# Performance work log

Measured on AMD Instinct MI355X. Metric: run time of the kernel, lower is better.

## Reference

```python
import jax, jax.numpy as jnp
import numpy as np

N_EMBD = 768
N_HEAD = 12
HEAD_DIM = N_EMBD // N_HEAD


def setup_inputs() -> dict:
    key = jax.random.key(0)
    k0, k1, k2, k3, k4 = jax.random.split(key, 5)
    B, T, C = 2, 4096, N_EMBD
    x = jax.random.normal(k0, (B, T, C), dtype=jnp.float32)
    # c_attn: Linear(C, 3C); c_proj: Linear(C, C). torch Linear: y = x @ W.T + b
    s = 1.0 / np.sqrt(C)
    W_attn = jax.random.uniform(k1, (3 * C, C), dtype=jnp.float32, minval=-s, maxval=s)
    b_attn = jax.random.uniform(k2, (3 * C,), dtype=jnp.float32, minval=-s, maxval=s)
    W_proj = jax.random.uniform(k3, (C, C), dtype=jnp.float32, minval=-s, maxval=s)
    b_proj = jax.random.uniform(k4, (C,), dtype=jnp.float32, minval=-s, maxval=s)
    return {"x": x, "W_attn": W_attn, "b_attn": b_attn, "W_proj": W_proj, "b_proj": b_proj}


def reference(x, W_attn, b_attn, W_proj, b_proj):
    B, T, C = x.shape
    H, D = N_HEAD, HEAD_DIM
    qkv = x @ W_attn.T + b_attn                      # [B,T,3C]
    q, k, v = jnp.split(qkv, 3, axis=-1)
    # [B,T,C] -> [B,H,T,D]
    q = q.reshape(B, T, H, D).transpose(0, 2, 1, 3)
    k = k.reshape(B, T, H, D).transpose(0, 2, 1, 3)
    v = v.reshape(B, T, H, D).transpose(0, 2, 1, 3)
    scale = 1.0 / jnp.sqrt(jnp.asarray(D, dtype=x.dtype))
    att = jnp.einsum('bhqd,bhkd->bhqk', q, k) * scale  # [B,H,T,T]
    att = jax.nn.softmax(att, axis=-1)
    y = jnp.einsum('bhqk,bhkd->bhqd', att, v)          # [B,H,T,D]
    y = y.transpose(0, 2, 1, 3).reshape(B, T, C)
    return y @ W_proj.T + b_proj
```

## Files before the change

### kernel.cpp

```cpp
#include <hip/hip_runtime.h>
#include <stdint.h>
#include <stddef.h>

typedef __bf16 bf16_t;
typedef bf16_t bf16x4 __attribute__((ext_vector_type(4)));
typedef bf16_t bf16x8 __attribute__((ext_vector_type(8)));
typedef float  f32x4  __attribute__((ext_vector_type(4)));
typedef _Float16 f16_t;
typedef f16_t f16x2 __attribute__((ext_vector_type(2)));
typedef f16_t f16x4 __attribute__((ext_vector_type(4)));
typedef f16_t f16x8 __attribute__((ext_vector_type(8)));
typedef __fp16 fp16x2_raw __attribute__((ext_vector_type(2)));

__device__ __forceinline__ f16x2 pkrtz(float a, float b) {
    fp16x2_raw r = __builtin_amdgcn_cvt_pkrtz(a, b);
    union { fp16x2_raw r; f16x2 h; } u;
    u.r = r;
    return u.h;
}

#define MFMA_BF16_K32(a, b, c) __builtin_amdgcn_mfma_f32_16x16x32_bf16(a, b, c, 0, 0, 0)
#define MFMA_F16_K32(a, b, c)  __builtin_amdgcn_mfma_f32_16x16x32_f16(a, b, c, 0, 0, 0)

__device__ __forceinline__ void gload_lds16(const void* g, void* l) {
    __builtin_amdgcn_global_load_lds(
        (const __attribute__((address_space(1))) void*)g,
        (__attribute__((address_space(3))) void*)l,
        16, 0, 0);
}

#define NX 1572864
#define NWA 442368
#define NWP 147456
__global__ void cvt_all(const float* __restrict__ x, const float* __restrict__ Wa,
                        const float* __restrict__ Wp, bf16_t* __restrict__ xb,
                        bf16_t* __restrict__ Wab, bf16_t* __restrict__ Wpb) {
    int i = blockIdx.x * blockDim.x + threadIdx.x;
    const float4* src; bf16_t* dst; int j;
    if (i < NX)            { src = (const float4*)x;  dst = xb;  j = i; }
    else if (i < NX + NWA) { src = (const float4*)Wa; dst = Wab; j = i - NX; }
    else                   { src = (const float4*)Wp; dst = Wpb; j = i - NX - NWA; }
    float4 f = src[j];
    bf16x4 o = { (bf16_t)f.x, (bf16_t)f.y, (bf16_t)f.z, (bf16_t)f.w };
    ((bf16x4*)dst)[j] = o;
}

template <int KDIM>
__device__ __forceinline__ void gemm_mainloop(
    const bf16_t* __restrict__ A, const bf16_t* __restrict__ Bt,
    bf16_t* As, bf16_t* Bs, int m0, int n0, int wave, int lane, f32x4 acc[4][4])
{
    const int quad = lane >> 4, l15 = lane & 15;
    const int wm = ((wave >> 1) << 6), wn = ((wave & 1) << 6);

    const int srow = (wave << 4) + (lane >> 2);
    const int sw   = (((lane & 3) ^ ((srow >> 1) & 3)) << 3);
    const bf16_t* gA = A  + (size_t)(m0 + srow) * KDIM + sw;
    const bf16_t* gB = Bt + (size_t)(n0 + srow) * KDIM + sw;
    bf16_t* lA0 = As + wave * 512;
    bf16_t* lA1 = As + 2048 + wave * 512;
    bf16_t* lB0 = Bs + wave * 512;
    bf16_t* lB1 = Bs + 2048 + wave * 512;

    const int xorv = ((quad ^ ((l15 >> 1) & 3)) << 3);

    for (int k0 = 0; k0 < KDIM; k0 += 32) {
        __syncthreads();
        gload_lds16(gA + k0,                       lA0);
        gload_lds16(gA + (size_t)64 * KDIM + k0,   lA1);
        gload_lds16(gB + k0,                       lB0);
        gload_lds16(gB + (size_t)64 * KDIM + k0,   lB1);
        __syncthreads();

        bf16x8 af[4], bfr[4];
#pragma unroll
        for (int t = 0; t < 4; t++) {
            af[t]  = *(const bf16x8*)(As + (wm + t * 16 + l15) * 32 + xorv);
            bfr[t] = *(const bf16x8*)(Bs + (wn + t * 16 + l15) * 32 + xorv);
        }
#pragma unroll
        for (int mt = 0; mt < 4; mt++)
#pragma unroll
            for (int nt = 0; nt < 4; nt++)
                acc[mt][nt] = MFMA_BF16_K32(af[mt], bfr[nt], acc[mt][nt]);
    }
}

__global__ __launch_bounds__(256) void gemm_qkv(
    const bf16_t* __restrict__ A,
    const bf16_t* __restrict__ Bt,
    const float* __restrict__ bias,
    bf16_t* __restrict__ qo, bf16_t* __restrict__ ko, f16_t* __restrict__ vo)
{
    __shared__ bf16_t As[128 * 32];
    __shared__ bf16_t Bs[128 * 32];
    const int tid = threadIdx.x, wave = tid >> 6, lane = tid & 63;
    const int quad = lane >> 4, l15 = lane & 15;
    const int m0 = blockIdx.y * 128, n0 = blockIdx.x * 128;
    f32x4 acc[4][4] = {};
    gemm_mainloop<768>(A, Bt, As, Bs, m0, n0, wave, lane, acc);

    const int wm = ((wave >> 1) << 6), wn = ((wave & 1) << 6);
#pragma unroll
    for (int nt = 0; nt < 4; nt++) {
        const int cc = n0 + wn + nt * 16 + l15;
        const float bia = bias[cc];
        const int which = cc / 768;
        const int rem = cc - which * 768;
        const int h = rem >> 6, d = rem & 63;
        if (which < 2) {
            bf16_t* dst = (which == 0) ? qo : ko;
#pragma unroll
            for (int mt = 0; mt < 4; mt++) {
#pragma unroll
                for (int r = 0; r < 4; r++) {
                    const int row = m0 + wm + mt * 16 + quad * 4 + r;
                    const int b = row >> 12, t = row & 4095;
                    dst[((size_t)(b * 12 + h) * 4096 + t) * 64 + d] =
                        (bf16_t)(acc[mt][nt][r] + bia);
                }
            }
        } else {
#pragma unroll
            for (int mt = 0; mt < 4; mt++) {
                const int row0 = m0 + wm + mt * 16 + quad * 4;
                const int b = row0 >> 12, t0 = row0 & 4095;
                f16x4 ov = { (f16_t)(acc[mt][nt][0] + bia),
                             (f16_t)(acc[mt][nt][1] + bia),
                             (f16_t)(acc[mt][nt][2] + bia),
                             (f16_t)(acc[mt][nt][3] + bia) };
                *(f16x4*)(vo + ((size_t)(b * 12 + h) * 64 + d) * 4096 + t0) = ov;
            }
        }
    }
}

__global__ __launch_bounds__(256) void gemm_proj(
    const bf16_t* __restrict__ A,
    const bf16_t* __restrict__ Bt,
    const float* __restrict__ bias,
    float* __restrict__ out)
{
    __shared__ bf16_t As[128 * 32];
    __shared__ bf16_t Bs[128 * 32];
    const int tid = threadIdx.x, wave = tid >> 6, lane = tid & 63;
    const int quad = lane >> 4, l15 = lane & 15;
    const int m0 = blockIdx.y * 128, n0 = blockIdx.x * 128;
    f32x4 acc[4][4] = {};
    gemm_mainloop<768>(A, Bt, As, Bs, m0, n0, wave, lane, acc);

    const int wm = ((wave >> 1) << 6), wn = ((wave & 1) << 6);
#pragma unroll
    for (int nt = 0; nt < 4; nt++) {
        const int cc = n0 + wn + nt * 16 + l15;
        const float bia = bias[cc];
#pragma unroll
        for (int mt = 0; mt < 4; mt++) {
#pragma unroll
            for (int r = 0; r < 4; r++) {
                const int row = m0 + wm + mt * 16 + quad * 4 + r;
                out[(size_t)row * 768 + cc] = acc[mt][nt][r] + bia;
            }
        }
    }
}

#define QSCALE 0.1803368801f
#define SBAR()   __builtin_amdgcn_s_barrier()
#define SCHEDB() __builtin_amdgcn_sched_barrier(0)
#define WAITV(N) asm volatile("s_waitcnt vmcnt(" #N ")" ::: "memory")
__global__ __launch_bounds__(256, 3) void attn_fwd(
    const bf16_t* __restrict__ qg, const bf16_t* __restrict__ kg,
    const f16_t* __restrict__ vtg, bf16_t* __restrict__ y)
{
    __shared__ __align__(16) char smem[49152];
    bf16_t* Ks0 = (bf16_t*)(smem);
    bf16_t* Ks1 = (bf16_t*)(smem + 8192);
    bf16_t* Ks2 = (bf16_t*)(smem + 16384);
    bf16_t* Ks3 = (bf16_t*)(smem + 24576);
    f16_t*  Vt0 = (f16_t*)(smem + 32768);
    f16_t*  Vt1 = (f16_t*)(smem + 40960);
    float*  RedA = (float*)(smem);
    float*  RedB = (float*)(smem + 17408);
    float*  Psr  = (float*)(smem + 34816);
    float*  PsT  = (float*)(smem + 35840);

    const int tid = threadIdx.x, wave = tid >> 6, lane = tid & 63;
    const int quad = lane >> 4, l15 = lane & 15;

    const int blk = blockIdx.x;
    const int xcd = blk & 7;
    const int idx = blk >> 3;
    const int hl  = idx % 3;
    const int qt  = idx / 3;
    const int bh  = xcd * 3 + hl;
    const int b = bh / 12, h = bh - b * 12;
    const size_t base = (size_t)bh * 4096 * 64;

    bf16x8 qf[4][2];
#pragma unroll
    for (int qc = 0; qc < 4; qc++) {
        const int qrow = qt * 64 + qc * 16 + l15;
        qf[qc][0] = *(const bf16x8*)(qg + base + (size_t)qrow * 64 + quad * 8);
        qf[qc][1] = *(const bf16x8*)(qg + base + (size_t)qrow * 64 + 32 + quad * 8);
#pragma unroll
        for (int j = 0; j < 8; j++) {
            qf[qc][0][j] = (bf16_t)((float)qf[qc][0][j] * QSCALE);
            qf[qc][1][j] = (bf16_t)((float)qf[qc][1][j] * QSCALE);
        }
    }

    f32x4 O[4][4] = {};
    float psum[4] = {};
    const f16x2 one2 = { (f16_t)1.0f, (f16_t)1.0f };

    const int srow8 = tid >> 3;
    const int sc8   = (tid & 7) ^ (srow8 & 7);
    const int l8 = l15 & 7;
    const int w16 = wave << 4;
    const int ksoff = (quad ^ l8) << 3;
    const int vslot = ((wave << 1) | (quad >> 1)) ^ l8;
    const int q0off = (quad & 1) * 8;

    auto stage_k = [&](const bf16_t* kp_, bf16_t* Kd) {
#pragma unroll
        for (int i = 0; i < 2; i++)
            gload_lds16(kp_ + (i * 32 + srow8) * 64 + sc8 * 8, Kd + (i * 256 + tid) * 8);
    };
    auto stage_v = [&](const f16_t* vp_, f16_t* Vd) {
#pragma unroll
        for (int i = 0; i < 2; i++)
            gload_lds16(vp_ + (size_t)(i * 32 + srow8) * 4096 + sc8 * 8, Vd + (i * 256 + tid) * 8);
    };

    auto compute_pair = [&](const bf16_t* ksA, const bf16_t* ksB) {
        const bf16_t* krA = ksA + (w16 + l15) * 64;
        const bf16_t* krB = ksB + (w16 + l15) * 64;
        bf16x8 kfA0 = *(const bf16x8*)(krA + ksoff);
        bf16x8 kfA1 = *(const bf16x8*)(krA + (ksoff ^ 32));
        bf16x8 kfB0 = *(const bf16x8*)(krB + ksoff);
        bf16x8 kfB1 = *(const bf16x8*)(krB + (ksoff ^ 32));
        f32x4 scA[4], scB[4];
        __builtin_amdgcn_s_setprio(1);
#pragma unroll
        for (int qc = 0; qc < 4; qc++) {
            f32x4 s = {};
            s = MFMA_BF16_K32(kfA0, qf[qc][0], s);
            s = MFMA_BF16_K32(kfA1, qf[qc][1], s);
            scA[qc] = s;
        }
#pragma unroll
        for (int qc = 0; qc < 4; qc++) {
            f32x4 s = {};
            s = MFMA_BF16_K32(kfB0, qf[qc][0], s);
            s = MFMA_BF16_K32(kfB1, qf[qc][1], s);
            scB[qc] = s;
        }
        __builtin_amdgcn_s_setprio(0);
        f16x8 pf8[4];
#pragma unroll
        for (int qc = 0; qc < 4; qc++) {
            float a0 = __builtin_amdgcn_exp2f(scA[qc][0]);
            float a1 = __builtin_amdgcn_exp2f(scA[qc][1]);
            float a2 = __builtin_amdgcn_exp2f(scA[qc][2]);
            float a3 = __builtin_amdgcn_exp2f(scA[qc][3]);
            float b0 = __builtin_amdgcn_exp2f(scB[qc][0]);
            float b1 = __builtin_amdgcn_exp2f(scB[qc][1]);
            float b2 = __builtin_amdgcn_exp2f(scB[qc][2]);
            float b3 = __builtin_amdgcn_exp2f(scB[qc][3]);
            f16x2 loA = pkrtz(a0, a1);
            f16x2 hiA = pkrtz(a2, a3);
            f16x2 loB = pkrtz(b0, b1);
            f16x2 hiB = pkrtz(b2, b3);
            psum[qc] = __builtin_amdgcn_fdot2(loA, one2, psum[qc], false);
            psum[qc] = __builtin_amdgcn_fdot2(hiA, one2, psum[qc], false);
            psum[qc] = __builtin_amdgcn_fdot2(loB, one2, psum[qc], false);
            psum[qc] = __builtin_amdgcn_fdot2(hiB, one2, psum[qc], false);
            union { f16x8 v; f16x2 h[4]; } u;
            u.h[0] = loA; u.h[1] = hiA; u.h[2] = loB; u.h[3] = hiB;
            pf8[qc] = u.v;
        }
        WAITV(4);
        SBAR();
        SCHEDB();
        __builtin_amdgcn_s_setprio(1);
#pragma unroll
        for (int dt = 0; dt < 4; dt++) {
            const char* vrA = (const char*)(Vt0 + (dt * 16 + l15) * 64);
            const char* vrB = (const char*)(Vt1 + (dt * 16 + l15) * 64);
            f16x4 vA = *(const f16x4*)(vrA + vslot * 16 + q0off);
            f16x4 vB = *(const f16x4*)(vrB + vslot * 16 + q0off);
            union { f16x8 v; f16x4 h[2]; } uv;
            uv.h[0] = vA; uv.h[1] = vB;
#pragma unroll
            for (int qc = 0; qc < 4; qc++)
                O[dt][qc] = MFMA_F16_K32(uv.v, pf8[qc], O[dt][qc]);
        }
        __builtin_amdgcn_s_setprio(0);
    };

    const bf16_t* kp = kg + base;
    const f16_t*  vp = vtg + base;
    stage_k(kp, Ks0); stage_k(kp + 4096, Ks1);
    stage_v(vp, Vt0); stage_v(vp + 64, Vt1);
    WAITV(0);
    SBAR();
    SCHEDB();
    stage_k(kp + 8192, Ks2); stage_k(kp + 12288, Ks3);
    for (int p = 0; p < 32; p++) {
        compute_pair((p & 1) ? Ks2 : Ks0, (p & 1) ? Ks3 : Ks1);
        WAITV(0);
        SBAR();
        SCHEDB();
        if (p < 31) {
            const f16_t* vn = vp + (size_t)(p + 1) * 128;
            stage_v(vn, Vt0); stage_v(vn + 64, Vt1);
            SCHEDB();
            const int kt = (p + 2 < 32) ? (p + 2) : 31;
            const bf16_t* kn = kp + (size_t)kt * 8192;
            stage_k(kn, (p & 1) ? Ks2 : Ks0);
            stage_k(kn + 4096, (p & 1) ? Ks3 : Ks1);
        }
    }

#pragma unroll
    for (int qc = 0; qc < 4; qc++) {
        psum[qc] += __shfl_xor(psum[qc], 16, 64);
        psum[qc] += __shfl_xor(psum[qc], 32, 64);
    }
    __syncthreads();
    if (wave == 2) {
#pragma unroll
        for (int dt = 0; dt < 4; dt++)
#pragma unroll
            for (int qc = 0; qc < 4; qc++)
                *(f32x4*)(RedA + (qc * 16 + l15) * 68 + dt * 16 + quad * 4) = O[dt][qc];
    } else if (wave == 3) {
#pragma unroll
        for (int dt = 0; dt < 4; dt++)
#pragma unroll
            for (int qc = 0; qc < 4; qc++)
                *(f32x4*)(RedB + (qc * 16 + l15) * 68 + dt * 16 + quad * 4) = O[dt][qc];
    }
    if (quad == 0) {
#pragma unroll
        for (int qc = 0; qc < 4; qc++) Psr[wave * 64 + qc * 16 + l15] = psum[qc];
    }
    __syncthreads();
    if (wave == 0) {
#pragma unroll
        for (int dt = 0; dt < 4; dt++)
#pragma unroll
            for (int qc = 0; qc < 4; qc++)
                O[dt][qc] += *(const f32x4*)(RedA + (qc * 16 + l15) * 68 + dt * 16 + quad * 4);
    } else if (wave == 1) {
#pragma unroll
        for (int dt = 0; dt < 4; dt++)
#pragma unroll
            for (int qc = 0; qc < 4; qc++)
                O[dt][qc] += *(const f32x4*)(RedB + (qc * 16 + l15) * 68 + dt * 16 + quad * 4);
    }
    __syncthreads();
    if (wave == 1) {
#pragma unroll
        for (int dt = 0; dt < 4; dt++)
#pragma unroll
            for (int qc = 0; qc < 4; qc++)
                *(f32x4*)(RedA + (qc * 16 + l15) * 68 + dt * 16 + quad * 4) = O[dt][qc];
    } else if (wave == 3) {
        PsT[lane] = Psr[lane] + Psr[64 + lane] + Psr[128 + lane] + Psr[192 + lane];
    }
    __syncthreads();
    if (wave == 0) {
#pragma unroll
        for (int qc = 0; qc < 4; qc++) {
            const float rcp = 1.0f / PsT[qc * 16 + l15];
            const int t = qt * 64 + qc * 16 + l15;
            bf16_t* yr = y + ((size_t)b * 4096 + t) * 768 + h * 64 + quad * 4;
#pragma unroll
            for (int dt = 0; dt < 4; dt++) {
                f32x4 o4 = O[dt][qc] +
                    *(const f32x4*)(RedA + (qc * 16 + l15) * 68 + dt * 16 + quad * 4);
                bf16x4 ov = { (bf16_t)(o4[0] * rcp), (bf16_t)(o4[1] * rcp),
                              (bf16_t)(o4[2] * rcp), (bf16_t)(o4[3] * rcp) };
                *(bf16x4*)(yr + dt * 16) = ov;
            }
        }
    }
}

extern "C" void kernel_launch(void* const* d_in, const int* in_sizes, int n_in,
                              void* d_out, int out_size, void* d_ws, size_t ws_size,
                              hipStream_t stream) {
    const float* x  = (const float*)d_in[0];
    const float* Wa = (const float*)d_in[1];
    const float* ba = (const float*)d_in[2];
    const float* Wp = (const float*)d_in[3];
    const float* bp = (const float*)d_in[4];
    float* out = (float*)d_out;

    char* ws = (char*)d_ws;
    bf16_t* xb  = (bf16_t*)(ws);
    bf16_t* Wab = (bf16_t*)(ws + 12582912);
    bf16_t* Wpb = (bf16_t*)(ws + 16121856);
    bf16_t* qb  = (bf16_t*)(ws + 17301504);
    bf16_t* kb  = (bf16_t*)(ws + 29884416);
    f16_t*  vtb = (f16_t*)(ws + 42467328);
    bf16_t* yb  = (bf16_t*)(ws + 55050240);

    cvt_all<<<8448, 256, 0, stream>>>(x, Wa, Wp, xb, Wab, Wpb);
    gemm_qkv <<<dim3(18, 64), 256, 0, stream>>>(xb, Wab, ba, qb, kb, vtb);
    attn_fwd <<<1536, 256, 0, stream>>>(qb, kb, vtb, yb);
    gemm_proj<<<dim3( 6, 64), 256, 0, stream>>>(yb, Wpb, bp, out);
}
```

Before: 272.7 us.

## Share staged K/V tiles across two query groups in 512-thread attention blocks

The attention kernel now runs with 512 threads per block, as two groups of four waves. Each group handles its own 64-row query tile while both share the same K and V tiles staged in LDS, so each staged tile feeds twice as many queries and global/LDS staging traffic per query is halved. Staging loads drop to one 16-byte load per thread, the vmcnt wait is adjusted to match, and the cross-wave output reduction runs once per query group, serialized with extra barriers. The launch bound is raised to (512, 4), which caps register allocation hard for a kernel holding large O accumulators and could cause spills. The requested occupancy may also exceed what the LDS footprint allows.

```diff
diff --git a/kernel.cpp b/kernel.cpp
--- a/kernel.cpp
+++ b/kernel.cpp
@@ -169,7 +169,7 @@
 #define SBAR()   __builtin_amdgcn_s_barrier()
 #define SCHEDB() __builtin_amdgcn_sched_barrier(0)
 #define WAITV(N) asm volatile("s_waitcnt vmcnt(" #N ")" ::: "memory")
-__global__ __launch_bounds__(256, 3) void attn_fwd(
+__global__ __launch_bounds__(512, 4) void attn_fwd(
     const bf16_t* __restrict__ qg, const bf16_t* __restrict__ kg,
     const f16_t* __restrict__ vtg, bf16_t* __restrict__ y)
 {
@@ -187,6 +187,8 @@
 
     const int tid = threadIdx.x, wave = tid >> 6, lane = tid & 63;
     const int quad = lane >> 4, l15 = lane & 15;
+    const int kwave = wave & 3;
+    const int qgrp  = wave >> 2;
 
     const int blk = blockIdx.x;
     const int xcd = blk & 7;
@@ -200,7 +202,7 @@
     bf16x8 qf[4][2];
 #pragma unroll
     for (int qc = 0; qc < 4; qc++) {
-        const int qrow = qt * 64 + qc * 16 + l15;
+        const int qrow = qt * 128 + qgrp * 64 + qc * 16 + l15;
         qf[qc][0] = *(const bf16x8*)(qg + base + (size_t)qrow * 64 + quad * 8);
         qf[qc][1] = *(const bf16x8*)(qg + base + (size_t)qrow * 64 + 32 + quad * 8);
 #pragma unroll
@@ -217,20 +219,16 @@
     const int srow8 = tid >> 3;
     const int sc8   = (tid & 7) ^ (srow8 & 7);
     const int l8 = l15 & 7;
-    const int w16 = wave << 4;
+    const int w16 = kwave << 4;
     const int ksoff = (quad ^ l8) << 3;
-    const int vslot = ((wave << 1) | (quad >> 1)) ^ l8;
+    const int vslot = ((kwave << 1) | (quad >> 1)) ^ l8;
     const int q0off = (quad & 1) * 8;
 
     auto stage_k = [&](const bf16_t* kp_, bf16_t* Kd) {
-#pragma unroll
-        for (int i = 0; i < 2; i++)
-            gload_lds16(kp_ + (i * 32 + srow8) * 64 + sc8 * 8, Kd + (i * 256 + tid) * 8);
+        gload_lds16(kp_ + srow8 * 64 + sc8 * 8, Kd + tid * 8);
     };
     auto stage_v = [&](const f16_t* vp_, f16_t* Vd) {
-#pragma unroll
-        for (int i = 0; i < 2; i++)
-            gload_lds16(vp_ + (size_t)(i * 32 + srow8) * 4096 + sc8 * 8, Vd + (i * 256 + tid) * 8);
+        gload_lds16(vp_ + (size_t)srow8 * 4096 + sc8 * 8, Vd + tid * 8);
     };
 
     auto compute_pair = [&](const bf16_t* ksA, const bf16_t* ksB) {
@@ -280,7 +278,7 @@
             u.h[0] = loA; u.h[1] = hiA; u.h[2] = loB; u.h[3] = hiB;
             pf8[qc] = u.v;
         }
-        WAITV(4);
+        WAITV(2);
         SBAR();
         SCHEDB();
         __builtin_amdgcn_s_setprio(1);
@@ -328,62 +326,65 @@
         psum[qc] += __shfl_xor(psum[qc], 16, 64);
         psum[qc] += __shfl_xor(psum[qc], 32, 64);
     }
-    __syncthreads();
-    if (wave == 2) {
-#pragma unroll
-        for (int dt = 0; dt < 4; dt++)
-#pragma unroll
-            for (int qc = 0; qc < 4; qc++)
-                *(f32x4*)(RedA + (qc * 16 + l15) * 68 + dt * 16 + quad * 4) = O[dt][qc];
-    } else if (wave == 3) {
-#pragma unroll
-        for (int dt = 0; dt < 4; dt++)
-#pragma unroll
-            for (int qc = 0; qc < 4; qc++)
-                *(f32x4*)(RedB + (qc * 16 + l15) * 68 + dt * 16 + quad * 4) = O[dt][qc];
-    }
-    if (quad == 0) {
-#pragma unroll
-        for (int qc = 0; qc < 4; qc++) Psr[wave * 64 + qc * 16 + l15] = psum[qc];
-    }
-    __syncthreads();
-    if (wave == 0) {
-#pragma unroll
-        for (int dt = 0; dt < 4; dt++)
-#pragma unroll
-            for (int qc = 0; qc < 4; qc++)
-                O[dt][qc] += *(const f32x4*)(RedA + (qc * 16 + l15) * 68 + dt * 16 + quad * 4);
-    } else if (wave == 1) {
-#pragma unroll
-        for (int dt = 0; dt < 4; dt++)
-#pragma unroll
-            for (int qc = 0; qc < 4; qc++)
-                O[dt][qc] += *(const f32x4*)(RedB + (qc * 16 + l15) * 68 + dt * 16 + quad * 4);
-    }
-    __syncthreads();
-    if (wave == 1) {
-#pragma unroll
-        for (int dt = 0; dt < 4; dt++)
-#pragma unroll
-            for (int qc = 0; qc < 4; qc++)
-                *(f32x4*)(RedA + (qc * 16 + l15) * 68 + dt * 16 + quad * 4) = O[dt][qc];
-    } else if (wave == 3) {
-        PsT[lane] = Psr[lane] + Psr[64 + lane] + Psr[128 + lane] + Psr[192 + lane];
-    }
-    __syncthreads();
-    if (wave == 0) {
-#pragma unroll
-        for (int qc = 0; qc < 4; qc++) {
-            const float rcp = 1.0f / PsT[qc * 16 + l15];
-            const int t = qt * 64 + qc * 16 + l15;
-            bf16_t* yr = y + ((size_t)b * 4096 + t) * 768 + h * 64 + quad * 4;
-#pragma unroll
-            for (int dt = 0; dt < 4; dt++) {
-                f32x4 o4 = O[dt][qc] +
-                    *(const f32x4*)(RedA + (qc * 16 + l15) * 68 + dt * 16 + quad * 4);
-                bf16x4 ov = { (bf16_t)(o4[0] * rcp), (bf16_t)(o4[1] * rcp),
-                              (bf16_t)(o4[2] * rcp), (bf16_t)(o4[3] * rcp) };
-                *(bf16x4*)(yr + dt * 16) = ov;
+    for (int g = 0; g < 2; g++) {
+        const int lw = (qgrp == g) ? kwave : -1;
+        __syncthreads();
+        if (lw == 2) {
+#pragma unroll
+            for (int dt = 0; dt < 4; dt++)
+#pragma unroll
+                for (int qc = 0; qc < 4; qc++)
+                    *(f32x4*)(RedA + (qc * 16 + l15) * 68 + dt * 16 + quad * 4) = O[dt][qc];
+        } else if (lw == 3) {
+#pragma unroll
+            for (int dt = 0; dt < 4; dt++)
+#pragma unroll
+                for (int qc = 0; qc < 4; qc++)
+                    *(f32x4*)(RedB + (qc * 16 + l15) * 68 + dt * 16 + quad * 4) = O[dt][qc];
+        }
+        if (lw >= 0 && quad == 0) {
+#pragma unroll
+            for (int qc = 0; qc < 4; qc++) Psr[lw * 64 + qc * 16 + l15] = psum[qc];
+        }
+        __syncthreads();
+        if (lw == 0) {
+#pragma unroll
+            for (int dt = 0; dt < 4; dt++)
+#pragma unroll
+                for (int qc = 0; qc < 4; qc++)
+                    O[dt][qc] += *(const f32x4*)(RedA + (qc * 16 + l15) * 68 + dt * 16 + quad * 4);
+        } else if (lw == 1) {
+#pragma unroll
+            for (int dt = 0; dt < 4; dt++)
+#pragma unroll
+                for (int qc = 0; qc < 4; qc++)
+                    O[dt][qc] += *(const f32x4*)(RedB + (qc * 16 + l15) * 68 + dt * 16 + quad * 4);
+        }
+        __syncthreads();
+        if (lw == 1) {
+#pragma unroll
+            for (int dt = 0; dt < 4; dt++)
+#pragma unroll
+                for (int qc = 0; qc < 4; qc++)
+                    *(f32x4*)(RedA + (qc * 16 + l15) * 68 + dt * 16 + quad * 4) = O[dt][qc];
+        } else if (lw == 3) {
+            PsT[lane] = Psr[lane] + Psr[64 + lane] + Psr[128 + lane] + Psr[192 + lane];
+        }
+        __syncthreads();
+        if (lw == 0) {
+#pragma unroll
+            for (int qc = 0; qc < 4; qc++) {
+                const float rcp = 1.0f / PsT[qc * 16 + l15];
+                const int t = qt * 128 + g * 64 + qc * 16 + l15;
+                bf16_t* yr = y + ((size_t)b * 4096 + t) * 768 + h * 64 + quad * 4;
+#pragma unroll
+                for (int dt = 0; dt < 4; dt++) {
+                    f32x4 o4 = O[dt][qc] +
+                        *(const f32x4*)(RedA + (qc * 16 + l15) * 68 + dt * 16 + quad * 4);
+                    bf16x4 ov = { (bf16_t)(o4[0] * rcp), (bf16_t)(o4[1] * rcp),
+                                  (bf16_t)(o4[2] * rcp), (bf16_t)(o4[3] * rcp) };
+                    *(bf16x4*)(yr + dt * 16) = ov;
+                }
             }
         }
     }
@@ -410,6 +411,6 @@
 
     cvt_all<<<8448, 256, 0, stream>>>(x, Wa, Wp, xb, Wab, Wpb);
     gemm_qkv <<<dim3(18, 64), 256, 0, stream>>>(xb, Wab, ba, qb, kb, vtb);
-    attn_fwd <<<1536, 256, 0, stream>>>(qb, kb, vtb, yb);
+    attn_fwd <<<768, 512, 0, stream>>>(qb, kb, vtb, yb);
     gemm_proj<<<dim3( 6, 64), 256, 0, stream>>>(yb, Wpb, bp, out);
 }
```

Result: slower. 497.4 us (+82.4%).
